# Kernel tuning notes

Hardware: AMD Instinct MI355X
Metric: run time of the kernel (lower is better)

The kernel has to match this reference:

```python
import jax, jax.numpy as jnp
import numpy as np

B, S, C, H, D = 2, 2048, 1024, 16, 64  # hidden C must equal H*D (value is a reshape of key_states)


def setup_inputs() -> dict:
    key = jax.random.key(0)
    ks = jax.random.split(key, 7)
    query_states = jax.random.normal(ks[0], (B, S, C), dtype=jnp.float32)
    key_states = jax.random.normal(ks[1], (B, S, C), dtype=jnp.float32)
    attention_mask = jax.random.randint(ks[2], (B, 1, 1, S), 0, 2).astype(jnp.int32)
    Wq = jax.random.normal(ks[3], (C, H, D), dtype=jnp.float32) * 0.02
    bq = jnp.zeros((H, D), dtype=jnp.float32)
    Wk = jax.random.normal(ks[4], (C, H, D), dtype=jnp.float32) * 0.02
    bk = jnp.zeros((H, D), dtype=jnp.float32)
    return {
        "query_states": query_states,
        "key_states": key_states,
        "attention_mask": attention_mask,
        "Wq": Wq,
        "bq": bq,
        "Wk": Wk,
        "bk": bk,
    }


def reference(query_states, key_states, attention_mask, Wq, bq, Wk, bk):
    # EinsumDense 'abc,cde->abde' with bias on 'de'
    q = jnp.einsum("bsc,chd->bshd", query_states, Wq) + bq  # [B,S,H,D]
    k = jnp.einsum("bsc,chd->bshd", key_states, Wk) + bk    # [B,S,H,D]
    # value is just key_states reshaped into head layout (no projection!)
    v = key_states.reshape(k.shape)                          # [B,S,H,D]
    # scale query by 1/sqrt(dk)
    q = q * jax.lax.rsqrt(jnp.asarray(D, q.dtype))
    # 'aecd,abcd->acbe': a=batch, c=head, b=query pos, e=key pos
    scores = jnp.einsum("bkhd,bqhd->bhqk", k, q)             # [B,H,Sq,Sk]
    mask = (1.0 - attention_mask.astype(scores.dtype)) * -10000.0
    scores = scores + mask
    probs = jax.nn.softmax(scores, axis=-1)
    # dropout is identity at training=False (default)
    # 'acbe,aecd->abcd': weighted sum of values over key positions
    out = jnp.einsum("bhqk,bkhd->bqhd", probs, v)            # [B,S,H,D]
    return out
```

## Files before the change

kernel.cpp:

```cpp
#include <hip/hip_runtime.h>

#define BSZ 2
#define SEQ 2048
#define CH  1024
#define NH  16
#define HD  64
#define LOG2E 1.4426950408889634f
#define MASKC (-14426.950408889634f)

typedef short  bf16x8 __attribute__((ext_vector_type(8)));
typedef short  bf16x4 __attribute__((ext_vector_type(4)));
typedef float  f32x4  __attribute__((ext_vector_type(4)));

__device__ __forceinline__ short f2bf(float f) {
    union { float f; unsigned u; } v; v.f = f;
    unsigned r = v.u + 0x7FFFu + ((v.u >> 16) & 1u);
    return (short)(r >> 16);
}
__device__ __forceinline__ short f2bf_fast(float f) {
    union { float f; unsigned u; } v; v.f = f;
    return (short)((v.u + 0x8000u) >> 16);
}
__device__ __forceinline__ float exp2_hw(float x) {
#if __has_builtin(__builtin_amdgcn_exp2f)
    return __builtin_amdgcn_exp2f(x);
#else
    float r;
    asm volatile("v_exp_f32 %0, %1\n\ts_nop 1" : "=v"(r) : "v"(x));
    return r;
#endif
}

#if __has_builtin(__builtin_amdgcn_mfma_f32_16x16x16bf16_1k)
__device__ __forceinline__ f32x4 mfma16x16x16(bf16x4 a, bf16x4 b, f32x4 c) {
    return __builtin_amdgcn_mfma_f32_16x16x16bf16_1k(a, b, c, 0, 0, 0);
}
#else
__device__ __forceinline__ f32x4 mfma16x16x16(bf16x4 a, bf16x4 b, f32x4 c) {
    f32x4 d;
    asm("v_mfma_f32_16x16x16_bf16 %0, %1, %2, %3"
        : "=v"(d) : "v"(a), "v"(b), "v"(c));
    return d;
}
#endif

__global__ __launch_bounds__(256) void prep(
    const float* __restrict__ query, const float* __restrict__ key,
    const float* __restrict__ Wq, const float* __restrict__ Wk,
    short* __restrict__ qc, short* __restrict__ kc,
    short* __restrict__ wtq, short* __restrict__ wtk,
    short* __restrict__ vtr)
{
    __shared__ float tile[64][65];
    const int bid = blockIdx.x;
    const int tid = threadIdx.x;

    if (bid < 4096) {
        const float* s = (bid < 2048) ? query : key;
        short*       d = (bid < 2048) ? qc : kc;
        long i = ((long)(bid & 2047) * 256 + tid) * 8;
        float4 v0 = *(const float4*)&s[i];
        float4 v1 = *(const float4*)&s[i + 4];
        bf16x8 o;
        o[0] = f2bf(v0.x); o[1] = f2bf(v0.y); o[2] = f2bf(v0.z); o[3] = f2bf(v0.w);
        o[4] = f2bf(v1.x); o[5] = f2bf(v1.y); o[6] = f2bf(v1.z); o[7] = f2bf(v1.w);
        *(bf16x8*)&d[i] = o;
        return;
    }

    const float* s; short* d;
    int r0, c0, srs, drs;
    if (bid < 4608) {
        int t = bid - 4096;
        s   = (t < 256) ? Wq : Wk;
        d   = (t < 256) ? wtq : wtk;
        t  &= 255;
        r0  = (t >> 4) * 64;
        c0  = (t & 15) * 64;
        srs = CH; drs = CH;
    } else {
        int t = bid - 4608;
        int z = t >> 5;
        int sy = t & 31;
        s   = key + (long)(z >> 4) * SEQ * CH + (long)(z & 15) * HD;
        d   = vtr + (long)z * HD * SEQ;
        r0  = sy * 64;
        c0  = 0;
        srs = CH; drs = SEQ;
    }

    const int r  = tid >> 2;
    const int c4 = (tid & 3) << 4;
    #pragma unroll
    for (int i = 0; i < 16; i += 4) {
        float4 v = *(const float4*)&s[(long)(r0 + r) * srs + c0 + c4 + i];
        tile[r][c4 + i + 0] = v.x;
        tile[r][c4 + i + 1] = v.y;
        tile[r][c4 + i + 2] = v.z;
        tile[r][c4 + i + 3] = v.w;
    }
    __syncthreads();
    bf16x8 o0, o1;
    #pragma unroll
    for (int i = 0; i < 8; i++) o0[i] = f2bf(tile[c4 + i][r]);
    #pragma unroll
    for (int i = 0; i < 8; i++) o1[i] = f2bf(tile[c4 + 8 + i][r]);
    *(bf16x8*)&d[(long)(c0 + r) * drs + r0 + c4 + 0] = o0;
    *(bf16x8*)&d[(long)(c0 + r) * drs + r0 + c4 + 8] = o1;
}

__global__ __launch_bounds__(256, 2) void proj_mfma(
    const short* __restrict__ Xq, const short* __restrict__ Xk,
    const short* __restrict__ Wtq, const short* __restrict__ Wtk,
    const float* __restrict__ bq_, const float* __restrict__ bk_,
    short* __restrict__ Yq, short* __restrict__ Yk)
{
    __shared__ short At[2][128 * 72];
    __shared__ short Bt[2][128 * 72];
    const int zz = blockIdx.z;
    const short* X    = zz ? Xk  : Xq;
    const short* Wt   = zz ? Wtk : Wtq;
    const float* bias = zz ? bk_ : bq_;
    short*       Y    = zz ? Yk  : Yq;
    const float scale = zz ? 1.0f : (0.125f * LOG2E);

    const int tid  = threadIdx.x;
    const int lane = tid & 63, w = tid >> 6;
    const int quad = lane >> 4, t16 = lane & 15;
    const int m0 = blockIdx.y * 128, n0 = blockIdx.x * 128;
    const int srow = tid >> 1;
    const int shalf = (tid & 1) * 32;

    f32x4 acc[4][4];
    #pragma unroll
    for (int i = 0; i < 4; i++)
        #pragma unroll
        for (int j = 0; j < 4; j++)
            acc[i][j] = (f32x4){0.f, 0.f, 0.f, 0.f};

    const int M0 = (w >> 1) * 64, N0 = (w & 1) * 64;
    const int NIT = CH / 64;

    bf16x8 ar[4], br[4];
    #pragma unroll
    for (int c = 0; c < 4; c++) {
        ar[c] = *(const bf16x8*)&X [(long)(m0 + srow) * CH + shalf + 8 * c];
        br[c] = *(const bf16x8*)&Wt[(long)(n0 + srow) * CH + shalf + 8 * c];
    }
    #pragma unroll
    for (int c = 0; c < 4; c++) {
        *(bf16x8*)&At[0][srow * 72 + shalf + 8 * c] = ar[c];
        *(bf16x8*)&Bt[0][srow * 72 + shalf + 8 * c] = br[c];
    }
    #pragma unroll
    for (int c = 0; c < 4; c++) {
        ar[c] = *(const bf16x8*)&X [(long)(m0 + srow) * CH + 64 + shalf + 8 * c];
        br[c] = *(const bf16x8*)&Wt[(long)(n0 + srow) * CH + 64 + shalf + 8 * c];
    }
    __syncthreads();

    for (int it = 0; it < NIT; it++) {
        const int buf = it & 1;
        if (it + 1 < NIT) {
            #pragma unroll
            for (int c = 0; c < 4; c++) {
                *(bf16x8*)&At[buf ^ 1][srow * 72 + shalf + 8 * c] = ar[c];
                *(bf16x8*)&Bt[buf ^ 1][srow * 72 + shalf + 8 * c] = br[c];
            }
            if (it + 2 < NIT) {
                const long ko = (long)(it + 2) * 64;
                #pragma unroll
                for (int c = 0; c < 4; c++) {
                    ar[c] = *(const bf16x8*)&X [(long)(m0 + srow) * CH + ko + shalf + 8 * c];
                    br[c] = *(const bf16x8*)&Wt[(long)(n0 + srow) * CH + ko + shalf + 8 * c];
                }
            }
        }

        #pragma unroll
        for (int kk = 0; kk < 2; kk++) {
            bf16x8 af[4], bw[4];
            #pragma unroll
            for (int im = 0; im < 4; im++)
                af[im] = *(bf16x8*)&At[buf][(M0 + 16 * im + t16) * 72 + kk * 32 + quad * 8];
            #pragma unroll
            for (int jn = 0; jn < 4; jn++)
                bw[jn] = *(bf16x8*)&Bt[buf][(N0 + 16 * jn + t16) * 72 + kk * 32 + quad * 8];
            #pragma unroll
            for (int im = 0; im < 4; im++)
                #pragma unroll
                for (int jn = 0; jn < 4; jn++)
                    acc[im][jn] = __builtin_amdgcn_mfma_f32_16x16x32_bf16(
                        af[im], bw[jn], acc[im][jn], 0, 0, 0);
        }
        __syncthreads();
    }

    #pragma unroll
    for (int jn = 0; jn < 4; jn++) {
        float bs = bias[n0 + N0 + 16 * jn + t16];
        #pragma unroll
        for (int im = 0; im < 4; im++)
            #pragma unroll
            for (int reg = 0; reg < 4; reg++) {
                float y = (acc[im][jn][reg] + bs) * scale;
                Y[(long)(m0 + M0 + 16 * im + 4 * quad + reg) * (NH * HD)
                  + n0 + N0 + 16 * jn + t16] = f2bf(y);
            }
    }
}

__global__ __launch_bounds__(256, 2) void attn_mfma(
    const short* __restrict__ qp,
    const short* __restrict__ kp,
    const short* __restrict__ vt,
    const int*   __restrict__ amask,
    float* __restrict__ out)
{
    __shared__ short Kt[2][64 * 72];
    __shared__ short Vt[2][64 * 72];

    const int qt0 = blockIdx.x * 128;
    const int h   = blockIdx.y;
    const int b   = blockIdx.z;
    const int tid = threadIdx.x;
    const int lane = tid & 63, w = tid >> 6;
    const int quad = lane >> 4, t16 = lane & 15;

    bf16x8 qf[2][2];
    #pragma unroll
    for (int qm = 0; qm < 2; qm++)
        #pragma unroll
        for (int ds = 0; ds < 2; ds++)
            qf[qm][ds] = *(const bf16x8*)&qp[
                (long)(b * SEQ + qt0 + w * 32 + qm * 16 + t16) * CH
                + h * HD + ds * 32 + quad * 8];

    f32x4 oa[4][2];
    float l_r[2];
    #pragma unroll
    for (int dt = 0; dt < 4; dt++)
        #pragma unroll
        for (int qm = 0; qm < 2; qm++)
            oa[dt][qm] = (f32x4){0.f, 0.f, 0.f, 0.f};
    l_r[0] = l_r[1] = 0.f;

    const int srow  = tid >> 2;
    const int scol  = (tid & 3) * 16;
    const long kbase = (long)(b * SEQ) * CH + h * HD;
    const long vbase = ((long)(b * NH + h) * HD) * SEQ;
    const int NIT = SEQ / 64;

    bf16x8 kr[2], vr[2];
    #pragma unroll
    for (int c = 0; c < 2; c++) {
        kr[c] = *(const bf16x8*)&kp[kbase + (long)srow * CH + scol + 8 * c];
        vr[c] = *(const bf16x8*)&vt[vbase + (long)srow * SEQ + scol + 8 * c];
    }
    #pragma unroll
    for (int c = 0; c < 2; c++) {
        *(bf16x8*)&Kt[0][srow * 72 + scol + 8 * c] = kr[c];
        *(bf16x8*)&Vt[0][srow * 72 + scol + 8 * c] = vr[c];
    }
    #pragma unroll
    for (int c = 0; c < 2; c++) {
        kr[c] = *(const bf16x8*)&kp[kbase + (long)(64 + srow) * CH + scol + 8 * c];
        vr[c] = *(const bf16x8*)&vt[vbase + (long)srow * SEQ + 64 + scol + 8 * c];
    }
    __syncthreads();

    for (int it = 0; it < NIT; it++) {
        const int buf = it & 1;
        const int kt0 = it * 64;

        if (it + 1 < NIT) {
            #pragma unroll
            for (int c = 0; c < 2; c++) {
                *(bf16x8*)&Kt[buf ^ 1][srow * 72 + scol + 8 * c] = kr[c];
                *(bf16x8*)&Vt[buf ^ 1][srow * 72 + scol + 8 * c] = vr[c];
            }
            if (it + 2 < NIT) {
                const int kn = kt0 + 128;
                #pragma unroll
                for (int c = 0; c < 2; c++) {
                    kr[c] = *(const bf16x8*)&kp[kbase + (long)(kn + srow) * CH + scol + 8 * c];
                    vr[c] = *(const bf16x8*)&vt[vbase + (long)srow * SEQ + kn + scol + 8 * c];
                }
            }
        }

        float4 mv4[4];
        #pragma unroll
        for (int jt = 0; jt < 4; jt++) {
            int4 a4 = *(const int4*)&amask[b * SEQ + kt0 + jt * 16 + quad * 4];
            mv4[jt].x = a4.x ? 0.f : MASKC;
            mv4[jt].y = a4.y ? 0.f : MASKC;
            mv4[jt].z = a4.z ? 0.f : MASKC;
            mv4[jt].w = a4.w ? 0.f : MASKC;
        }

        f32x4 sa[2][4];
        #pragma unroll
        for (int qm = 0; qm < 2; qm++)
            #pragma unroll
            for (int jt = 0; jt < 4; jt++)
                sa[qm][jt] = (f32x4){mv4[jt].x, mv4[jt].y, mv4[jt].z, mv4[jt].w};
        #pragma unroll
        for (int ds = 0; ds < 2; ds++) {
            bf16x8 kb[4];
            #pragma unroll
            for (int jt = 0; jt < 4; jt++)
                kb[jt] = *(bf16x8*)&Kt[buf][(jt * 16 + t16) * 72 + ds * 32 + quad * 8];
            __builtin_amdgcn_s_setprio(1);
            #pragma unroll
            for (int qm = 0; qm < 2; qm++)
                #pragma unroll
                for (int jt = 0; jt < 4; jt++)
                    sa[qm][jt] = __builtin_amdgcn_mfma_f32_16x16x32_bf16(
                        kb[jt], qf[qm][ds], sa[qm][jt], 0, 0, 0);
            __builtin_amdgcn_s_setprio(0);
        }

        bf16x4 pb[2][4];
        #pragma unroll
        for (int qm = 0; qm < 2; qm++)
            #pragma unroll
            for (int jt = 0; jt < 4; jt++) {
                float p0 = exp2_hw(sa[qm][jt][0]);
                float p1 = exp2_hw(sa[qm][jt][1]);
                float p2 = exp2_hw(sa[qm][jt][2]);
                float p3 = exp2_hw(sa[qm][jt][3]);
                l_r[qm] += (p0 + p1) + (p2 + p3);
                bf16x4 pk;
                pk[0] = f2bf_fast(p0); pk[1] = f2bf_fast(p1);
                pk[2] = f2bf_fast(p2); pk[3] = f2bf_fast(p3);
                pb[qm][jt] = pk;
            }

        #pragma unroll
        for (int jt = 0; jt < 4; jt++) {
            bf16x4 va[4];
            #pragma unroll
            for (int dt = 0; dt < 4; dt++)
                va[dt] = *(bf16x4*)&Vt[buf][(dt * 16 + t16) * 72 + jt * 16 + quad * 4];
            __builtin_amdgcn_s_setprio(1);
            #pragma unroll
            for (int dt = 0; dt < 4; dt++)
                #pragma unroll
                for (int qm = 0; qm < 2; qm++)
                    oa[dt][qm] = mfma16x16x16(va[dt], pb[qm][jt], oa[dt][qm]);
            __builtin_amdgcn_s_setprio(0);
        }
        __syncthreads();
    }

    #pragma unroll
    for (int qm = 0; qm < 2; qm++) {
        float l = l_r[qm];
        l += __shfl_xor(l, 16, 64);
        l += __shfl_xor(l, 32, 64);
        float inv = 1.0f / l;
        int q = qt0 + w * 32 + qm * 16 + t16;
        #pragma unroll
        for (int dt = 0; dt < 4; dt++) {
            f32x4 o = oa[dt][qm];
            float4 st = {o[0] * inv, o[1] * inv, o[2] * inv, o[3] * inv};
            *(float4*)&out[((long)(b * SEQ + q) * NH + h) * HD + dt * 16 + quad * 4] = st;
        }
    }
}

extern "C" void kernel_launch(void* const* d_in, const int* in_sizes, int n_in,
                              void* d_out, int out_size, void* d_ws, size_t ws_size,
                              hipStream_t stream) {
    const float* query = (const float*)d_in[0];
    const float* key   = (const float*)d_in[1];
    const int*   amask = (const int*)d_in[2];
    const float* Wq    = (const float*)d_in[3];
    const float* bq    = (const float*)d_in[4];
    const float* Wk    = (const float*)d_in[5];
    const float* bk    = (const float*)d_in[6];
    float* out = (float*)d_out;

    char* ws = (char*)d_ws;
    const long MB = 1024 * 1024;
    short* qc  = (short*)(ws + 0 * MB);
    short* kc  = (short*)(ws + 8 * MB);
    short* qp  = (short*)(ws + 16 * MB);
    short* kp  = (short*)(ws + 24 * MB);
    short* vtr = (short*)(ws + 32 * MB);
    short* wtq = (short*)(ws + 40 * MB);
    short* wtk = (short*)(ws + 42 * MB);

    prep<<<dim3(5632), 256, 0, stream>>>(query, key, Wq, Wk, qc, kc, wtq, wtk, vtr);

    dim3 pgrid((NH * HD) / 128, (BSZ * SEQ) / 128, 2);
    proj_mfma<<<pgrid, 256, 0, stream>>>(qc, kc, wtq, wtk, bq, bk, qp, kp);

    dim3 agrid(SEQ / 128, NH, BSZ);
    attn_mfma<<<agrid, 256, 0, stream>>>(qp, kp, vtr, amask, out);
}
```

Baseline: 177.3 us.

## Split attention over key halves with larger query tiles and a combine pass

Each attention block now processes 256 queries (64 per wave) instead of 128 and covers only half of the key sequence, so every K/V tile loaded into shared memory serves twice as many query rows. Because the grid is doubled along the key dimension, the total block count stays the same. Unnormalized partial outputs and row sums are written to workspace, and a new combine kernel adds the two halves and normalizes them. This trades extra global writes and reads of the output plus one more kernel launch for less K/V traffic per query. Register pressure also rises, since each wave now holds 4x4 score and accumulator tiles, which may limit occupancy.

Result: slower. 182.2 us (+2.7%).

```diff
diff --git a/kernel.cpp b/kernel.cpp
--- a/kernel.cpp
+++ b/kernel.cpp
@@ -215,47 +215,52 @@
     const short* __restrict__ kp,
     const short* __restrict__ vt,
     const int*   __restrict__ amask,
-    float* __restrict__ out)
+    float* __restrict__ out,
+    float* __restrict__ op1,
+    float* __restrict__ lp0,
+    float* __restrict__ lp1)
 {
     __shared__ short Kt[2][64 * 72];
     __shared__ short Vt[2][64 * 72];
 
-    const int qt0 = blockIdx.x * 128;
+    const int qt0 = blockIdx.x * 256;
     const int h   = blockIdx.y;
-    const int b   = blockIdx.z;
+    const int b   = blockIdx.z >> 1;
+    const int ks  = blockIdx.z & 1;
+    const int koff = ks * (SEQ / 2);
     const int tid = threadIdx.x;
     const int lane = tid & 63, w = tid >> 6;
     const int quad = lane >> 4, t16 = lane & 15;
 
-    bf16x8 qf[2][2];
-    #pragma unroll
-    for (int qm = 0; qm < 2; qm++)
+    bf16x8 qf[4][2];
+    #pragma unroll
+    for (int qm = 0; qm < 4; qm++)
         #pragma unroll
         for (int ds = 0; ds < 2; ds++)
             qf[qm][ds] = *(const bf16x8*)&qp[
-                (long)(b * SEQ + qt0 + w * 32 + qm * 16 + t16) * CH
+                (long)(b * SEQ + qt0 + w * 64 + qm * 16 + t16) * CH
                 + h * HD + ds * 32 + quad * 8];
 
-    f32x4 oa[4][2];
-    float l_r[2];
+    f32x4 oa[4][4];
+    float l_r[4];
     #pragma unroll
     for (int dt = 0; dt < 4; dt++)
         #pragma unroll
-        for (int qm = 0; qm < 2; qm++)
+        for (int qm = 0; qm < 4; qm++)
             oa[dt][qm] = (f32x4){0.f, 0.f, 0.f, 0.f};
-    l_r[0] = l_r[1] = 0.f;
+    l_r[0] = l_r[1] = l_r[2] = l_r[3] = 0.f;
 
     const int srow  = tid >> 2;
     const int scol  = (tid & 3) * 16;
     const long kbase = (long)(b * SEQ) * CH + h * HD;
     const long vbase = ((long)(b * NH + h) * HD) * SEQ;
-    const int NIT = SEQ / 64;
+    const int NIT = (SEQ / 2) / 64;
 
     bf16x8 kr[2], vr[2];
     #pragma unroll
     for (int c = 0; c < 2; c++) {
-        kr[c] = *(const bf16x8*)&kp[kbase + (long)srow * CH + scol + 8 * c];
-        vr[c] = *(const bf16x8*)&vt[vbase + (long)srow * SEQ + scol + 8 * c];
+        kr[c] = *(const bf16x8*)&kp[kbase + (long)(koff + srow) * CH + scol + 8 * c];
+        vr[c] = *(const bf16x8*)&vt[vbase + (long)srow * SEQ + koff + scol + 8 * c];
     }
     #pragma unroll
     for (int c = 0; c < 2; c++) {
@@ -264,8 +269,8 @@
     }
     #pragma unroll
     for (int c = 0; c < 2; c++) {
-        kr[c] = *(const bf16x8*)&kp[kbase + (long)(64 + srow) * CH + scol + 8 * c];
-        vr[c] = *(const bf16x8*)&vt[vbase + (long)srow * SEQ + 64 + scol + 8 * c];
+        kr[c] = *(const bf16x8*)&kp[kbase + (long)(koff + 64 + srow) * CH + scol + 8 * c];
+        vr[c] = *(const bf16x8*)&vt[vbase + (long)srow * SEQ + koff + 64 + scol + 8 * c];
     }
     __syncthreads();
 
@@ -283,8 +288,8 @@
                 const int kn = kt0 + 128;
                 #pragma unroll
                 for (int c = 0; c < 2; c++) {
-                    kr[c] = *(const bf16x8*)&kp[kbase + (long)(kn + srow) * CH + scol + 8 * c];
-                    vr[c] = *(const bf16x8*)&vt[vbase + (long)srow * SEQ + kn + scol + 8 * c];
+                    kr[c] = *(const bf16x8*)&kp[kbase + (long)(koff + kn + srow) * CH + scol + 8 * c];
+                    vr[c] = *(const bf16x8*)&vt[vbase + (long)srow * SEQ + koff + kn + scol + 8 * c];
                 }
             }
         }
@@ -292,16 +297,16 @@
         float4 mv4[4];
         #pragma unroll
         for (int jt = 0; jt < 4; jt++) {
-            int4 a4 = *(const int4*)&amask[b * SEQ + kt0 + jt * 16 + quad * 4];
+            int4 a4 = *(const int4*)&amask[b * SEQ + koff + kt0 + jt * 16 + quad * 4];
             mv4[jt].x = a4.x ? 0.f : MASKC;
             mv4[jt].y = a4.y ? 0.f : MASKC;
             mv4[jt].z = a4.z ? 0.f : MASKC;
             mv4[jt].w = a4.w ? 0.f : MASKC;
         }
 
-        f32x4 sa[2][4];
-        #pragma unroll
-        for (int qm = 0; qm < 2; qm++)
+        f32x4 sa[4][4];
+        #pragma unroll
+        for (int qm = 0; qm < 4; qm++)
             #pragma unroll
             for (int jt = 0; jt < 4; jt++)
                 sa[qm][jt] = (f32x4){mv4[jt].x, mv4[jt].y, mv4[jt].z, mv4[jt].w};
@@ -313,7 +318,7 @@
                 kb[jt] = *(bf16x8*)&Kt[buf][(jt * 16 + t16) * 72 + ds * 32 + quad * 8];
             __builtin_amdgcn_s_setprio(1);
             #pragma unroll
-            for (int qm = 0; qm < 2; qm++)
+            for (int qm = 0; qm < 4; qm++)
                 #pragma unroll
                 for (int jt = 0; jt < 4; jt++)
                     sa[qm][jt] = __builtin_amdgcn_mfma_f32_16x16x32_bf16(
@@ -321,11 +326,11 @@
             __builtin_amdgcn_s_setprio(0);
         }
 
-        bf16x4 pb[2][4];
-        #pragma unroll
-        for (int qm = 0; qm < 2; qm++)
-            #pragma unroll
-            for (int jt = 0; jt < 4; jt++) {
+        #pragma unroll
+        for (int jt = 0; jt < 4; jt++) {
+            bf16x4 pbq[4];
+            #pragma unroll
+            for (int qm = 0; qm < 4; qm++) {
                 float p0 = exp2_hw(sa[qm][jt][0]);
                 float p1 = exp2_hw(sa[qm][jt][1]);
                 float p2 = exp2_hw(sa[qm][jt][2]);
@@ -334,11 +339,8 @@
                 bf16x4 pk;
                 pk[0] = f2bf_fast(p0); pk[1] = f2bf_fast(p1);
                 pk[2] = f2bf_fast(p2); pk[3] = f2bf_fast(p3);
-                pb[qm][jt] = pk;
-            }
-
-        #pragma unroll
-        for (int jt = 0; jt < 4; jt++) {
+                pbq[qm] = pk;
+            }
             bf16x4 va[4];
             #pragma unroll
             for (int dt = 0; dt < 4; dt++)
@@ -347,27 +349,44 @@
             #pragma unroll
             for (int dt = 0; dt < 4; dt++)
                 #pragma unroll
-                for (int qm = 0; qm < 2; qm++)
-                    oa[dt][qm] = mfma16x16x16(va[dt], pb[qm][jt], oa[dt][qm]);
+                for (int qm = 0; qm < 4; qm++)
+                    oa[dt][qm] = mfma16x16x16(va[dt], pbq[qm], oa[dt][qm]);
             __builtin_amdgcn_s_setprio(0);
         }
         __syncthreads();
     }
 
-    #pragma unroll
-    for (int qm = 0; qm < 2; qm++) {
+    float* o_dst = ks ? op1 : out;
+    float* l_dst = ks ? lp1 : lp0;
+    #pragma unroll
+    for (int qm = 0; qm < 4; qm++) {
         float l = l_r[qm];
         l += __shfl_xor(l, 16, 64);
         l += __shfl_xor(l, 32, 64);
-        float inv = 1.0f / l;
-        int q = qt0 + w * 32 + qm * 16 + t16;
+        int q = qt0 + w * 64 + qm * 16 + t16;
+        if (quad == 0)
+            l_dst[(long)(b * SEQ + q) * NH + h] = l;
         #pragma unroll
         for (int dt = 0; dt < 4; dt++) {
             f32x4 o = oa[dt][qm];
-            float4 st = {o[0] * inv, o[1] * inv, o[2] * inv, o[3] * inv};
-            *(float4*)&out[((long)(b * SEQ + q) * NH + h) * HD + dt * 16 + quad * 4] = st;
-        }
-    }
+            float4 st = {o[0], o[1], o[2], o[3]};
+            *(float4*)&o_dst[((long)(b * SEQ + q) * NH + h) * HD + dt * 16 + quad * 4] = st;
+        }
+    }
+}
+
+__global__ __launch_bounds__(256) void combine(
+    const float* __restrict__ op1, const float* __restrict__ lp0,
+    const float* __restrict__ lp1, float* __restrict__ out)
+{
+    long i = ((long)blockIdx.x * 256 + threadIdx.x) * 4;
+    long bshq = i >> 6;
+    float4 a = *(const float4*)&out[i];
+    float4 c = *(const float4*)&op1[i];
+    float inv = 1.0f / (lp0[bshq] + lp1[bshq]);
+    float4 r = {(a.x + c.x) * inv, (a.y + c.y) * inv,
+                (a.z + c.z) * inv, (a.w + c.w) * inv};
+    *(float4*)&out[i] = r;
 }
 
 extern "C" void kernel_launch(void* const* d_in, const int* in_sizes, int n_in,
@@ -391,12 +410,17 @@
     short* vtr = (short*)(ws + 32 * MB);
     short* wtq = (short*)(ws + 40 * MB);
     short* wtk = (short*)(ws + 42 * MB);
+    float* op1 = (float*)(ws + 44 * MB);
+    float* lp0 = (float*)(ws + 60 * MB);
+    float* lp1 = (float*)(ws + 61 * MB);
 
     prep<<<dim3(5632), 256, 0, stream>>>(query, key, Wq, Wk, qc, kc, wtq, wtk, vtr);
 
     dim3 pgrid((NH * HD) / 128, (BSZ * SEQ) / 128, 2);
     proj_mfma<<<pgrid, 256, 0, stream>>>(qc, kc, wtq, wtk, bq, bk, qp, kp);
 
-    dim3 agrid(SEQ / 128, NH, BSZ);
-    attn_mfma<<<agrid, 256, 0, stream>>>(qp, kp, vtr, amask, out);
-}
+    dim3 agrid(SEQ / 256, NH, BSZ * 2);
+    attn_mfma<<<agrid, 256, 0, stream>>>(qp, kp, vtr, amask, out, op1, lp0, lp1);
+
+    combine<<<dim3(4096), 256, 0, stream>>>(op1, lp0, lp1, out);
+}
```

## Remap blocks per XCD for L2 reuse, stage mask in LDS, interleave softmax with PV

Applied to the files above, without the earlier changes.

Both the projection and attention kernels now use a flat 1D grid and remap block IDs so that blocks landing on the same XCD share operand rows (same head/batch or same M tile), improving L2 locality on the multi-die MI355X. The attention kernel precomputes the additive mask for the whole sequence into shared memory once instead of reloading and converting it from global memory every tile. The exp/convert of probabilities is interleaved per key subtile with the PV MFMAs to shorten register live ranges. This adds 8KB of LDS per block, which may affect occupancy, and the mask staging relies on the existing barrier before first use.

Result: faster. 170.8 us (-3.7%).

```diff
diff --git a/kernel.cpp b/kernel.cpp
--- a/kernel.cpp
+++ b/kernel.cpp
@@ -117,7 +117,14 @@
 {
     __shared__ short At[2][128 * 72];
     __shared__ short Bt[2][128 * 72];
-    const int zz = blockIdx.z;
+
+    const int bid  = blockIdx.x;
+    const int g    = bid >> 3, xcd = bid & 7;
+    const int pair = ((g >> 3) << 3) | xcd;
+    const int xt   = g & 7;
+    const int yy   = pair >> 1;
+    const int zz   = pair & 1;
+
     const short* X    = zz ? Xk  : Xq;
     const short* Wt   = zz ? Wtk : Wtq;
     const float* bias = zz ? bk_ : bq_;
@@ -127,7 +134,7 @@
     const int tid  = threadIdx.x;
     const int lane = tid & 63, w = tid >> 6;
     const int quad = lane >> 4, t16 = lane & 15;
-    const int m0 = blockIdx.y * 128, n0 = blockIdx.x * 128;
+    const int m0 = yy * 128, n0 = xt * 128;
     const int srow = tid >> 1;
     const int shalf = (tid & 1) * 32;
 
@@ -219,13 +226,30 @@
 {
     __shared__ short Kt[2][64 * 72];
     __shared__ short Vt[2][64 * 72];
-
-    const int qt0 = blockIdx.x * 128;
-    const int h   = blockIdx.y;
-    const int b   = blockIdx.z;
+    __shared__ float Msk[SEQ];
+
+    const int bid = blockIdx.x;
+    const int g   = bid >> 3, xcd = bid & 7;
+    const int hb  = ((g >> 4) << 3) | xcd;
+    const int qt  = g & 15;
+
+    const int qt0 = qt * 128;
+    const int h   = hb & 15;
+    const int b   = hb >> 4;
     const int tid = threadIdx.x;
     const int lane = tid & 63, w = tid >> 6;
     const int quad = lane >> 4, t16 = lane & 15;
+
+    {
+        int4 a0 = *(const int4*)&amask[b * SEQ + tid * 8];
+        int4 a1 = *(const int4*)&amask[b * SEQ + tid * 8 + 4];
+        float4 f0 = {a0.x ? 0.f : MASKC, a0.y ? 0.f : MASKC,
+                     a0.z ? 0.f : MASKC, a0.w ? 0.f : MASKC};
+        float4 f1 = {a1.x ? 0.f : MASKC, a1.y ? 0.f : MASKC,
+                     a1.z ? 0.f : MASKC, a1.w ? 0.f : MASKC};
+        *(float4*)&Msk[tid * 8]     = f0;
+        *(float4*)&Msk[tid * 8 + 4] = f1;
+    }
 
     bf16x8 qf[2][2];
     #pragma unroll
@@ -291,13 +315,8 @@
 
         float4 mv4[4];
         #pragma unroll
-        for (int jt = 0; jt < 4; jt++) {
-            int4 a4 = *(const int4*)&amask[b * SEQ + kt0 + jt * 16 + quad * 4];
-            mv4[jt].x = a4.x ? 0.f : MASKC;
-            mv4[jt].y = a4.y ? 0.f : MASKC;
-            mv4[jt].z = a4.z ? 0.f : MASKC;
-            mv4[jt].w = a4.w ? 0.f : MASKC;
-        }
+        for (int jt = 0; jt < 4; jt++)
+            mv4[jt] = *(const float4*)&Msk[kt0 + jt * 16 + quad * 4];
 
         f32x4 sa[2][4];
         #pragma unroll
@@ -321,11 +340,11 @@
             __builtin_amdgcn_s_setprio(0);
         }
 
-        bf16x4 pb[2][4];
-        #pragma unroll
-        for (int qm = 0; qm < 2; qm++)
-            #pragma unroll
-            for (int jt = 0; jt < 4; jt++) {
+        #pragma unroll
+        for (int jt = 0; jt < 4; jt++) {
+            bf16x4 pbq[2];
+            #pragma unroll
+            for (int qm = 0; qm < 2; qm++) {
                 float p0 = exp2_hw(sa[qm][jt][0]);
                 float p1 = exp2_hw(sa[qm][jt][1]);
                 float p2 = exp2_hw(sa[qm][jt][2]);
@@ -334,11 +353,8 @@
                 bf16x4 pk;
                 pk[0] = f2bf_fast(p0); pk[1] = f2bf_fast(p1);
                 pk[2] = f2bf_fast(p2); pk[3] = f2bf_fast(p3);
-                pb[qm][jt] = pk;
-            }
-
-        #pragma unroll
-        for (int jt = 0; jt < 4; jt++) {
+                pbq[qm] = pk;
+            }
             bf16x4 va[4];
             #pragma unroll
             for (int dt = 0; dt < 4; dt++)
@@ -348,7 +364,7 @@
             for (int dt = 0; dt < 4; dt++)
                 #pragma unroll
                 for (int qm = 0; qm < 2; qm++)
-                    oa[dt][qm] = mfma16x16x16(va[dt], pb[qm][jt], oa[dt][qm]);
+                    oa[dt][qm] = mfma16x16x16(va[dt], pbq[qm], oa[dt][qm]);
             __builtin_amdgcn_s_setprio(0);
         }
         __syncthreads();
@@ -394,9 +410,7 @@
 
     prep<<<dim3(5632), 256, 0, stream>>>(query, key, Wq, Wk, qc, kc, wtq, wtk, vtr);
 
-    dim3 pgrid((NH * HD) / 128, (BSZ * SEQ) / 128, 2);
-    proj_mfma<<<pgrid, 256, 0, stream>>>(qc, kc, wtq, wtk, bq, bk, qp, kp);
-
-    dim3 agrid(SEQ / 128, NH, BSZ);
-    attn_mfma<<<agrid, 256, 0, stream>>>(qp, kp, vtr, amask, out);
-}
+    proj_mfma<<<dim3(512), 256, 0, stream>>>(qc, kc, wtq, wtk, bq, bk, qp, kp);
+
+    attn_mfma<<<dim3(512), 256, 0, stream>>>(qp, kp, vtr, amask, out);
+}
```
